# Optimization experiments

Measured on AMD Instinct MI355X. Metric: run time of the kernel, lower is better.

Reference implementation:

```python
import jax, jax.numpy as jnp
import numpy as np

N_HEAD = 16


def setup_inputs() -> dict:
    key = jax.random.key(0)
    ks = jax.random.split(key, 9)
    B, T, C = 4, 2048, 1024
    s = 1.0 / np.sqrt(C)
    x = jax.random.normal(ks[0], (B, T, C), dtype=jnp.float32)
    Wq = jax.random.normal(ks[1], (C, C), dtype=jnp.float32) * s
    bq = jax.random.normal(ks[2], (C,), dtype=jnp.float32) * 0.01
    Wk = jax.random.normal(ks[3], (C, C), dtype=jnp.float32) * s
    bk = jax.random.normal(ks[4], (C,), dtype=jnp.float32) * 0.01
    Wv = jax.random.normal(ks[5], (C, C), dtype=jnp.float32) * s
    bv = jax.random.normal(ks[6], (C,), dtype=jnp.float32) * 0.01
    Wp = jax.random.normal(ks[7], (C, C), dtype=jnp.float32) * s
    bp = jax.random.normal(ks[8], (C,), dtype=jnp.float32) * 0.01
    return {"x": x, "Wq": Wq, "bq": bq, "Wk": Wk, "bk": bk,
            "Wv": Wv, "bv": bv, "Wp": Wp, "bp": bp}


def reference(x, Wq, bq, Wk, bk, Wv, bv, Wp, bp):
    B, T, C = x.shape
    H = N_HEAD
    d = C // H
    # projections (torch Linear: x @ W.T + b)
    q = (x @ Wq.T + bq).reshape(B, T, H, d)  # [B,T,H,d]
    k = (x @ Wk.T + bk).reshape(B, T, H, d)
    v = (x @ Wv.T + bv).reshape(B, T, H, d)
    scale = 1.0 / jnp.sqrt(jnp.asarray(d, dtype=x.dtype))
    # scores: [B,H,T,T]
    att = jnp.einsum('bqhd,bkhd->bhqk', q, k) * scale
    causal = jnp.tril(jnp.ones((T, T), dtype=bool))  # [T,T]
    att = jnp.where(causal[None, None], att, jnp.asarray(-jnp.inf, dtype=att.dtype))
    att = jax.nn.softmax(att, axis=-1)
    y = jnp.einsum('bhqk,bkhd->bqhd', att, v).reshape(B, T, C)
    return y @ Wp.T + bp
```

## Files before the change

### kernel.cpp

```cpp
#include <hip/hip_runtime.h>
#include <hip/hip_bf16.h>

typedef __attribute__((ext_vector_type(8))) short bf16x8;
typedef __attribute__((ext_vector_type(4))) float f32x4;

static constexpr int Tt = 2048;
static constexpr int Cc = 1024;
static constexpr int Dd = 64;
static constexpr int Mm = 8192;

static constexpr size_t XN = (size_t)Mm * Cc;
static constexpr size_t WN = (size_t)Cc * Cc;

__device__ __forceinline__ void async_copy16(void* lds, const void* g) {
  __builtin_amdgcn_global_load_lds(
      (const __attribute__((address_space(1))) void*)g,
      (__attribute__((address_space(3))) void*)lds, 16, 0, 0);
}

__device__ __forceinline__ unsigned short f2bf(float f) {
  union { float f; unsigned int u; } v; v.f = f;
  unsigned int r = (v.u + 0x7fffu + ((v.u >> 16) & 1u)) >> 16;
  return (unsigned short)r;
}
__device__ __forceinline__ unsigned int pack2bf(float f0, float f1) {
  unsigned int b0 = __float_as_uint(f0) + 0x8000u;
  unsigned int b1 = __float_as_uint(f1) + 0x8000u;
  return (b1 & 0xffff0000u) | (b0 >> 16);
}
__device__ __forceinline__ uint4 ldconv_f32(const float* p) {
  float4 lo = *(const float4*)p;
  float4 hi = *(const float4*)(p + 4);
  uint4 r;
  r.x = pack2bf(lo.x, lo.y);
  r.y = pack2bf(lo.z, lo.w);
  r.z = pack2bf(hi.x, hi.y);
  r.w = pack2bf(hi.z, hi.w);
  return r;
}

__global__ __launch_bounds__(256) void convert_all(
    const float* __restrict__ x, const float* __restrict__ wq,
    const float* __restrict__ wk, const float* __restrict__ wv,
    unsigned short* __restrict__ dst)
{
  const size_t i = ((size_t)blockIdx.x * 256 + threadIdx.x) * 8;
  const float* s; size_t off;
  if (i < XN)                { s = x;  off = 0; }
  else if (i < XN + WN)      { s = wq; off = XN; }
  else if (i < XN + 2 * WN)  { s = wk; off = XN + WN; }
  else                       { s = wv; off = XN + 2 * WN; }
  *(uint4*)(dst + i) = ldconv_f32(s + (i - off));
}

template <int MODE>
__device__ __forceinline__ void gemm_async_body(
    unsigned short* As, unsigned short* Bs,
    const unsigned short* __restrict__ A,
    const unsigned short* __restrict__ Bt,
    const float* __restrict__ bias,
    unsigned short* __restrict__ out, float mult)
{
  const int tid  = threadIdx.x;
  const int wave = tid >> 6;
  const int lane = tid & 63;
  const int m16  = lane & 15;
  const int quad = lane >> 4;
  const int row0 = blockIdx.x * 128;
  const int col0 = blockIdx.y * 128;
  const int wm = (wave >> 1) * 64;
  const int wn = (wave & 1) * 64;

  f32x4 acc[4][4] = {};

  const int c0 = tid, c1 = 256 + tid;
  const unsigned short* Ag0 = A  + (size_t)(row0 + (c0 >> 2)) * Cc + (c0 & 3) * 8;
  const unsigned short* Ag1 = A  + (size_t)(row0 + (c1 >> 2)) * Cc + (c1 & 3) * 8;
  const unsigned short* Bg0 = Bt + (size_t)(col0 + (c0 >> 2)) * Cc + (c0 & 3) * 8;
  const unsigned short* Bg1 = Bt + (size_t)(col0 + (c1 >> 2)) * Cc + (c1 & 3) * 8;
  char* Al0 = (char*)As + wave * 1024;
  char* Al1 = (char*)As + 4096 + wave * 1024;
  char* Bl0 = (char*)Bs + wave * 1024;
  char* Bl1 = (char*)Bs + 4096 + wave * 1024;

  for (int k0 = 0; k0 < Cc; k0 += 32) {
    __syncthreads();
    async_copy16(Al0, Ag0 + k0);
    async_copy16(Al1, Ag1 + k0);
    async_copy16(Bl0, Bg0 + k0);
    async_copy16(Bl1, Bg1 + k0);
    __syncthreads();
    bf16x8 af[4], bfr[4];
#pragma unroll
    for (int i = 0; i < 4; ++i)
      af[i] = *(const bf16x8*)(As + (wm + i * 16 + m16) * 32 + quad * 8);
#pragma unroll
    for (int j = 0; j < 4; ++j)
      bfr[j] = *(const bf16x8*)(Bs + (wn + j * 16 + m16) * 32 + quad * 8);
#pragma unroll
    for (int i = 0; i < 4; ++i)
#pragma unroll
      for (int j = 0; j < 4; ++j)
        acc[i][j] = __builtin_amdgcn_mfma_f32_16x16x32_bf16(af[i], bfr[j], acc[i][j], 0, 0, 0);
  }

#pragma unroll
  for (int i = 0; i < 4; ++i) {
    const int rbase = row0 + wm + i * 16 + quad * 4;
#pragma unroll
    for (int j = 0; j < 4; ++j) {
      const int col = col0 + wn + j * 16 + m16;
      const float bv = bias[col];
      if (MODE == 0) {
#pragma unroll
        for (int r = 0; r < 4; ++r)
          out[(size_t)(rbase + r) * Cc + col] = f2bf((acc[i][j][r] + bv) * mult);
      } else {
        const int t0 = rbase & (Tt - 1);
        const int b  = rbase >> 11;
        ushort4 pk;
        pk.x = f2bf(acc[i][j][0] + bv);
        pk.y = f2bf(acc[i][j][1] + bv);
        pk.z = f2bf(acc[i][j][2] + bv);
        pk.w = f2bf(acc[i][j][3] + bv);
        *(ushort4*)(out + (size_t)(b * Cc + col) * Tt + t0) = pk;
      }
    }
  }
}

__global__ __launch_bounds__(256) void qkv_gemm(
    const unsigned short* __restrict__ Xb,
    const unsigned short* __restrict__ Wqb, const float* __restrict__ bq,
    const unsigned short* __restrict__ Wkb, const float* __restrict__ bk,
    const unsigned short* __restrict__ Wvb, const float* __restrict__ bv,
    unsigned short* Qw, unsigned short* Kw, unsigned short* Vtw)
{
  __shared__ __align__(16) unsigned short smem[8192];
  const int z = blockIdx.z;
  if (z == 0)      gemm_async_body<0>(smem, smem + 4096, Xb, Wqb, bq, Qw, 0.125f * 1.44269504f);
  else if (z == 1) gemm_async_body<0>(smem, smem + 4096, Xb, Wkb, bk, Kw, 1.0f);
  else             gemm_async_body<1>(smem, smem + 4096, Xb, Wvb, bv, Vtw, 1.0f);
}

__global__ __launch_bounds__(256) void attn_pair(
    const unsigned short* __restrict__ Q,
    const unsigned short* __restrict__ Kg,
    const unsigned short* __restrict__ Vt,
    unsigned short* __restrict__ Y)
{
  __shared__ __align__(16) unsigned short KV[2 * 8192];

  const int tid  = threadIdx.x;
  const int wave = tid >> 6;
  const int lane = tid & 63;
  const int m16  = lane & 15;
  const int quad = lane >> 4;

  const int p  = blockIdx.x;
  const int bh = blockIdx.y;
  const int b = bh >> 4, h = bh & 15;

  const unsigned short* Kb = Kg + (size_t)(b * Tt) * Cc + h * Dd;
  const unsigned short* Vb = Vt + (size_t)(b * Cc + h * Dd) * Tt;

  const int maxH = 32 - 2 * p;
  const int TOT  = 34;
  const int chp  = quad ^ ((m16 >> 1) & 3);
  const int slA  = m16 + ((quad & 1) << 5);
  const int slB  = slA + 16;
  const int hi   = quad >> 1;

  int kkS[2], rrS[2], chdS[2];
#pragma unroll
  for (int ii = 0; ii < 2; ++ii) {
    const int cc = ii * 256 + tid;
    kkS[ii]  = cc >> 8;
    rrS[ii]  = (cc >> 2) & 63;
    chdS[ii] = (cc & 3) ^ ((rrS[ii] >> 1) & 3);
  }

  int sidx = 63 - 4 * p - wave;
  int qw = sidx * 32;
  int nk = (sidx >> 1) + 1;
  bf16x8 qf[2][2];
  {
    const unsigned short* Qb = Q + (size_t)(b * Tt + qw) * Cc + h * Dd;
#pragma unroll
    for (int s = 0; s < 2; ++s)
#pragma unroll
      for (int kk = 0; kk < 2; ++kk)
        qf[s][kk] = *(const bf16x8*)(Qb + (size_t)(s * 16 + m16) * Cc + kk * 32 + quad * 8);
  }
  f32x4 o[2][4] = {};
  float lsum[2] = {};

  auto writeout = [&](int qw_) {
#pragma unroll
    for (int s = 0; s < 2; ++s) {
      float l = lsum[s];
      l += __shfl_xor(l, 16, 64);
      l += __shfl_xor(l, 32, 64);
      const float inv = (l > 0.f) ? (1.0f / l) : 0.f;
      const int t = qw_ + s * 16 + m16;
      unsigned short* yp = Y + (size_t)(b * Tt + t) * Cc + h * Dd + quad * 4;
#pragma unroll
      for (int jn = 0; jn < 4; ++jn) {
        ushort4 pk;
        pk.x = f2bf(o[s][jn][0] * inv);
        pk.y = f2bf(o[s][jn][1] * inv);
        pk.z = f2bf(o[s][jn][2] * inv);
        pk.w = f2bf(o[s][jn][3] * inv);
        *(ushort4*)(yp + jn * 16) = pk;
      }
    }
  };

  {
    char* KbufB = (char*)KV;
    char* VbufB = KbufB + 8192;
#pragma unroll
    for (int ii = 0; ii < 2; ++ii) {
      async_copy16(KbufB + ii * 4096 + wave * 1024,
                   Kb + (size_t)rrS[ii] * Cc + kkS[ii] * 32 + chdS[ii] * 8);
      async_copy16(VbufB + ii * 4096 + wave * 1024,
                   Vb + (size_t)rrS[ii] * Tt + kkS[ii] * 32 + chdS[ii] * 8);
    }
  }

  for (int g = 0; g < TOT; ++g) {
    if (g == maxH) {
      writeout(qw);
      sidx = 4 * p + wave;
      qw = sidx * 32;
      nk = (sidx >> 1) + 1;
      const unsigned short* Qb = Q + (size_t)(b * Tt + qw) * Cc + h * Dd;
#pragma unroll
      for (int s = 0; s < 2; ++s) {
#pragma unroll
        for (int kk = 0; kk < 2; ++kk)
          qf[s][kk] = *(const bf16x8*)(Qb + (size_t)(s * 16 + m16) * Cc + kk * 32 + quad * 8);
#pragma unroll
        for (int jn = 0; jn < 4; ++jn)
          o[s][jn] = f32x4{0.f, 0.f, 0.f, 0.f};
        lsum[s] = 0.f;
      }
    }
    const int kt  = (g < maxH) ? g : g - maxH;
    const int k0  = kt * 64;
    const int buf = g & 1;

    __syncthreads();
    if (g + 1 < TOT) {
      const int g1  = g + 1;
      const int kt1 = (g1 < maxH) ? g1 : g1 - maxH;
      const int k1  = kt1 * 64;
      char* KbufB = (char*)KV + (buf ^ 1) * 16384;
      char* VbufB = KbufB + 8192;
#pragma unroll
      for (int ii = 0; ii < 2; ++ii) {
        async_copy16(KbufB + ii * 4096 + wave * 1024,
                     Kb + (size_t)(k1 + rrS[ii]) * Cc + kkS[ii] * 32 + chdS[ii] * 8);
        async_copy16(VbufB + ii * 4096 + wave * 1024,
                     Vb + (size_t)rrS[ii] * Tt + k1 + kkS[ii] * 32 + chdS[ii] * 8);
      }
    }

    if (kt < nk) {
      const unsigned short* Kbuf = KV + buf * 8192;
      const unsigned short* Vbuf = Kbuf + 4096;
      bf16x8 kf[2][4], vf[2][4];
#pragma unroll
      for (int kk = 0; kk < 2; ++kk)
#pragma unroll
        for (int jn = 0; jn < 4; ++jn) {
          kf[kk][jn] = *(const bf16x8*)(Kbuf + kk * 2048 + (jn * 16 + m16) * 32 + chp * 8);
          vf[kk][jn] = *(const bf16x8*)(Vbuf + kk * 2048 + (jn * 16 + m16) * 32 + chp * 8);
        }

#pragma unroll
      for (int s = 0; s < 2; ++s) {
        const int smin = qw + s * 16;
        if (k0 > smin + 15) continue;
        f32x4 sv[4] = {};
#pragma unroll
        for (int kk = 0; kk < 2; ++kk)
#pragma unroll
          for (int jn = 0; jn < 4; ++jn)
            sv[jn] = __builtin_amdgcn_mfma_f32_16x16x32_bf16(kf[kk][jn], qf[s][kk], sv[jn], 0, 0, 0);

        if (k0 + 63 <= smin) {
#pragma unroll
          for (int jn = 0; jn < 4; ++jn)
#pragma unroll
            for (int r = 0; r < 4; ++r) {
              const float pv = __builtin_exp2f(sv[jn][r]);
              sv[jn][r] = pv;
              lsum[s] += pv;
            }
        } else {
          const int qcol = smin + m16;
#pragma unroll
          for (int jn = 0; jn < 4; ++jn)
#pragma unroll
            for (int r = 0; r < 4; ++r) {
              const bool masked = (k0 + jn * 16 + quad * 4 + r > qcol);
              const float pv = masked ? 0.f : __builtin_exp2f(sv[jn][r]);
              sv[jn][r] = pv;
              lsum[s] += pv;
            }
        }
        unsigned int P2[4][2];
#pragma unroll
        for (int jn = 0; jn < 4; ++jn) {
          P2[jn][0] = pack2bf(sv[jn][0], sv[jn][1]);
          P2[jn][1] = pack2bf(sv[jn][2], sv[jn][3]);
        }
#pragma unroll
        for (int kk = 0; kk < 2; ++kk) {
          const int a0 = __shfl((int)P2[2 * kk][0],     slA, 64);
          const int b0 = __shfl((int)P2[2 * kk + 1][0], slA, 64);
          const int a1 = __shfl((int)P2[2 * kk][1],     slA, 64);
          const int b1 = __shfl((int)P2[2 * kk + 1][1], slA, 64);
          const int a2 = __shfl((int)P2[2 * kk][0],     slB, 64);
          const int b2 = __shfl((int)P2[2 * kk + 1][0], slB, 64);
          const int a3 = __shfl((int)P2[2 * kk][1],     slB, 64);
          const int b3 = __shfl((int)P2[2 * kk + 1][1], slB, 64);
          uint4 u;
          u.x = (unsigned int)(hi ? b0 : a0);
          u.y = (unsigned int)(hi ? b1 : a1);
          u.z = (unsigned int)(hi ? b2 : a2);
          u.w = (unsigned int)(hi ? b3 : a3);
          union { uint4 u4; bf16x8 bf; } cv; cv.u4 = u;
#pragma unroll
          for (int jn = 0; jn < 4; ++jn)
            o[s][jn] = __builtin_amdgcn_mfma_f32_16x16x32_bf16(vf[kk][jn], cv.bf, o[s][jn], 0, 0, 0);
        }
      }
    }
  }

  writeout(qw);
}

__global__ __launch_bounds__(256) void proj_gemm(
    const unsigned short* __restrict__ Y,
    const float* __restrict__ Wp, const float* __restrict__ bp,
    float* __restrict__ out)
{
  __shared__ __align__(16) unsigned short As[4096];
  __shared__ __align__(16) unsigned short Bs[4096];
  const int tid  = threadIdx.x;
  const int wave = tid >> 6;
  const int lane = tid & 63;
  const int m16  = lane & 15;
  const int quad = lane >> 4;
  const int row0 = blockIdx.x * 128;
  const int col0 = blockIdx.y * 128;
  const int wm = (wave >> 1) * 64;
  const int wn = (wave & 1) * 64;

  f32x4 acc[4][4] = {};

  const int c0 = tid, c1 = 256 + tid;
  const unsigned short* Ag0 = Y + (size_t)(row0 + (c0 >> 2)) * Cc + (c0 & 3) * 8;
  const unsigned short* Ag1 = Y + (size_t)(row0 + (c1 >> 2)) * Cc + (c1 & 3) * 8;
  const float* Bg0 = Wp + (size_t)(col0 + (c0 >> 2)) * Cc + (c0 & 3) * 8;
  const float* Bg1 = Wp + (size_t)(col0 + (c1 >> 2)) * Cc + (c1 & 3) * 8;
  char* Al0 = (char*)As + wave * 1024;
  char* Al1 = (char*)As + 4096 + wave * 1024;

  uint4 b0 = ldconv_f32(Bg0);
  uint4 b1 = ldconv_f32(Bg1);

  for (int k0 = 0; k0 < Cc; k0 += 32) {
    __syncthreads();
    async_copy16(Al0, Ag0 + k0);
    async_copy16(Al1, Ag1 + k0);
    *(uint4*)(Bs + (size_t)c0 * 8) = b0;
    *(uint4*)(Bs + (size_t)c1 * 8) = b1;
    __syncthreads();
    if (k0 + 32 < Cc) {
      b0 = ldconv_f32(Bg0 + k0 + 32);
      b1 = ldconv_f32(Bg1 + k0 + 32);
    }
    bf16x8 af[4], bfr[4];
#pragma unroll
    for (int i = 0; i < 4; ++i)
      af[i] = *(const bf16x8*)(As + (wm + i * 16 + m16) * 32 + quad * 8);
#pragma unroll
    for (int j = 0; j < 4; ++j)
      bfr[j] = *(const bf16x8*)(Bs + (wn + j * 16 + m16) * 32 + quad * 8);
#pragma unroll
    for (int i = 0; i < 4; ++i)
#pragma unroll
      for (int j = 0; j < 4; ++j)
        acc[i][j] = __builtin_amdgcn_mfma_f32_16x16x32_bf16(af[i], bfr[j], acc[i][j], 0, 0, 0);
  }

#pragma unroll
  for (int i = 0; i < 4; ++i) {
    const int rbase = row0 + wm + i * 16 + quad * 4;
#pragma unroll
    for (int j = 0; j < 4; ++j) {
      const int col = col0 + wn + j * 16 + m16;
      const float bv = bp[col];
#pragma unroll
      for (int r = 0; r < 4; ++r)
        out[(size_t)(rbase + r) * Cc + col] = acc[i][j][r] + bv;
    }
  }
}

extern "C" void kernel_launch(void* const* d_in, const int* in_sizes, int n_in,
                              void* d_out, int out_size, void* d_ws, size_t ws_size,
                              hipStream_t stream)
{
  const float* x  = (const float*)d_in[0];
  const float* Wq = (const float*)d_in[1];
  const float* bq = (const float*)d_in[2];
  const float* Wk = (const float*)d_in[3];
  const float* bk = (const float*)d_in[4];
  const float* Wv = (const float*)d_in[5];
  const float* bv = (const float*)d_in[6];
  const float* Wp = (const float*)d_in[7];
  const float* bp = (const float*)d_in[8];

  unsigned short* ws  = (unsigned short*)d_ws;
  unsigned short* Qw  = ws;
  unsigned short* Kw  = ws + (size_t)1 * XN;
  unsigned short* Vtw = ws + (size_t)2 * XN;
  unsigned short* Yw  = ws + (size_t)3 * XN;

  unsigned short* cvt = (unsigned short*)d_out;
  unsigned short* Xb  = cvt;
  unsigned short* Wqb = cvt + XN;
  unsigned short* Wkb = cvt + XN + WN;
  unsigned short* Wvb = cvt + XN + 2 * WN;
  float* out = (float*)d_out;

  convert_all<<<5632, 256, 0, stream>>>(x, Wq, Wk, Wv, cvt);
  qkv_gemm<<<dim3(64, 8, 3), 256, 0, stream>>>(Xb, Wqb, bq, Wkb, bk, Wvb, bv, Qw, Kw, Vtw);
  attn_pair<<<dim3(8, 64), 256, 0, stream>>>(Qw, Kw, Vtw, Yw);
  proj_gemm<<<dim3(64, 8), 256, 0, stream>>>(Yw, Wp, bp, out);
}
```

Before: 300.3 us.

## Replace paired causal attention blocks with per-strip blocks and permlane swaps

Each attention block previously handled a heavy and a light query strip pair in sequence (34 iterations). Now each block handles one strip, with 16 blocks per head launched largest-first. This gives more blocks for occupancy and removes the mid-loop strip switch. The P-matrix transpose now uses permlane32/16 swap intrinsics instead of eight shuffles plus selects. The row-sum uses a small vector accumulator, and launch bounds request 4 blocks per CU. The trade-off is uneven per-block work, which now relies on the hardware scheduler to balance the causal triangle.

```diff
diff --git a/kernel.cpp b/kernel.cpp
--- a/kernel.cpp
+++ b/kernel.cpp
@@ -143,7 +143,7 @@
   else             gemm_async_body<1>(smem, smem + 4096, Xb, Wvb, bv, Vtw, 1.0f);
 }
 
-__global__ __launch_bounds__(256) void attn_pair(
+__global__ __launch_bounds__(256, 4) void attn_strip(
     const unsigned short* __restrict__ Q,
     const unsigned short* __restrict__ Kg,
     const unsigned short* __restrict__ Vt,
@@ -157,19 +157,19 @@
   const int m16  = lane & 15;
   const int quad = lane >> 4;
 
-  const int p  = blockIdx.x;
+  const int pp = 15 - blockIdx.x;
   const int bh = blockIdx.y;
   const int b = bh >> 4, h = bh & 15;
 
   const unsigned short* Kb = Kg + (size_t)(b * Tt) * Cc + h * Dd;
   const unsigned short* Vb = Vt + (size_t)(b * Cc + h * Dd) * Tt;
 
-  const int maxH = 32 - 2 * p;
-  const int TOT  = 34;
+  const int sidx = 4 * pp + wave;
+  const int qw   = sidx * 32;
+  const int nk   = (sidx >> 1) + 1;
+  const int TOT  = 2 * pp + 2;
+
   const int chp  = quad ^ ((m16 >> 1) & 3);
-  const int slA  = m16 + ((quad & 1) << 5);
-  const int slB  = slA + 16;
-  const int hi   = quad >> 1;
 
   int kkS[2], rrS[2], chdS[2];
 #pragma unroll
@@ -180,9 +180,6 @@
     chdS[ii] = (cc & 3) ^ ((rrS[ii] >> 1) & 3);
   }
 
-  int sidx = 63 - 4 * p - wave;
-  int qw = sidx * 32;
-  int nk = (sidx >> 1) + 1;
   bf16x8 qf[2][2];
   {
     const unsigned short* Qb = Q + (size_t)(b * Tt + qw) * Cc + h * Dd;
@@ -194,27 +191,6 @@
   }
   f32x4 o[2][4] = {};
   float lsum[2] = {};
-
-  auto writeout = [&](int qw_) {
-#pragma unroll
-    for (int s = 0; s < 2; ++s) {
-      float l = lsum[s];
-      l += __shfl_xor(l, 16, 64);
-      l += __shfl_xor(l, 32, 64);
-      const float inv = (l > 0.f) ? (1.0f / l) : 0.f;
-      const int t = qw_ + s * 16 + m16;
-      unsigned short* yp = Y + (size_t)(b * Tt + t) * Cc + h * Dd + quad * 4;
-#pragma unroll
-      for (int jn = 0; jn < 4; ++jn) {
-        ushort4 pk;
-        pk.x = f2bf(o[s][jn][0] * inv);
-        pk.y = f2bf(o[s][jn][1] * inv);
-        pk.z = f2bf(o[s][jn][2] * inv);
-        pk.w = f2bf(o[s][jn][3] * inv);
-        *(ushort4*)(yp + jn * 16) = pk;
-      }
-    }
-  };
 
   {
     char* KbufB = (char*)KV;
@@ -229,32 +205,12 @@
   }
 
   for (int g = 0; g < TOT; ++g) {
-    if (g == maxH) {
-      writeout(qw);
-      sidx = 4 * p + wave;
-      qw = sidx * 32;
-      nk = (sidx >> 1) + 1;
-      const unsigned short* Qb = Q + (size_t)(b * Tt + qw) * Cc + h * Dd;
-#pragma unroll
-      for (int s = 0; s < 2; ++s) {
-#pragma unroll
-        for (int kk = 0; kk < 2; ++kk)
-          qf[s][kk] = *(const bf16x8*)(Qb + (size_t)(s * 16 + m16) * Cc + kk * 32 + quad * 8);
-#pragma unroll
-        for (int jn = 0; jn < 4; ++jn)
-          o[s][jn] = f32x4{0.f, 0.f, 0.f, 0.f};
-        lsum[s] = 0.f;
-      }
-    }
-    const int kt  = (g < maxH) ? g : g - maxH;
-    const int k0  = kt * 64;
+    const int k0  = g * 64;
     const int buf = g & 1;
 
     __syncthreads();
     if (g + 1 < TOT) {
-      const int g1  = g + 1;
-      const int kt1 = (g1 < maxH) ? g1 : g1 - maxH;
-      const int k1  = kt1 * 64;
+      const int k1 = (g + 1) * 64;
       char* KbufB = (char*)KV + (buf ^ 1) * 16384;
       char* VbufB = KbufB + 8192;
 #pragma unroll
@@ -266,7 +222,7 @@
       }
     }
 
-    if (kt < nk) {
+    if (g < nk) {
       const unsigned short* Kbuf = KV + buf * 8192;
       const unsigned short* Vbuf = Kbuf + 4096;
       bf16x8 kf[2][4], vf[2][4];
@@ -289,6 +245,7 @@
           for (int jn = 0; jn < 4; ++jn)
             sv[jn] = __builtin_amdgcn_mfma_f32_16x16x32_bf16(kf[kk][jn], qf[s][kk], sv[jn], 0, 0, 0);
 
+        f32x4 lacc = {0.f, 0.f, 0.f, 0.f};
         if (k0 + 63 <= smin) {
 #pragma unroll
           for (int jn = 0; jn < 4; ++jn)
@@ -296,7 +253,7 @@
             for (int r = 0; r < 4; ++r) {
               const float pv = __builtin_exp2f(sv[jn][r]);
               sv[jn][r] = pv;
-              lsum[s] += pv;
+              lacc[r] += pv;
             }
         } else {
           const int qcol = smin + m16;
@@ -307,9 +264,11 @@
               const bool masked = (k0 + jn * 16 + quad * 4 + r > qcol);
               const float pv = masked ? 0.f : __builtin_exp2f(sv[jn][r]);
               sv[jn][r] = pv;
-              lsum[s] += pv;
+              lacc[r] += pv;
             }
         }
+        lsum[s] += (lacc[0] + lacc[1]) + (lacc[2] + lacc[3]);
+
         unsigned int P2[4][2];
 #pragma unroll
         for (int jn = 0; jn < 4; ++jn) {
@@ -318,19 +277,15 @@
         }
 #pragma unroll
         for (int kk = 0; kk < 2; ++kk) {
-          const int a0 = __shfl((int)P2[2 * kk][0],     slA, 64);
-          const int b0 = __shfl((int)P2[2 * kk + 1][0], slA, 64);
-          const int a1 = __shfl((int)P2[2 * kk][1],     slA, 64);
-          const int b1 = __shfl((int)P2[2 * kk + 1][1], slA, 64);
-          const int a2 = __shfl((int)P2[2 * kk][0],     slB, 64);
-          const int b2 = __shfl((int)P2[2 * kk + 1][0], slB, 64);
-          const int a3 = __shfl((int)P2[2 * kk][1],     slB, 64);
-          const int b3 = __shfl((int)P2[2 * kk + 1][1], slB, 64);
+          auto r0 = __builtin_amdgcn_permlane32_swap(P2[2 * kk][0], P2[2 * kk + 1][0], false, false);
+          auto t0 = __builtin_amdgcn_permlane16_swap(r0[0], r0[1], false, false);
+          auto r1 = __builtin_amdgcn_permlane32_swap(P2[2 * kk][1], P2[2 * kk + 1][1], false, false);
+          auto t1 = __builtin_amdgcn_permlane16_swap(r1[0], r1[1], false, false);
           uint4 u;
-          u.x = (unsigned int)(hi ? b0 : a0);
-          u.y = (unsigned int)(hi ? b1 : a1);
-          u.z = (unsigned int)(hi ? b2 : a2);
-          u.w = (unsigned int)(hi ? b3 : a3);
+          u.x = t0[0];
+          u.y = t1[0];
+          u.z = t0[1];
+          u.w = t1[1];
           union { uint4 u4; bf16x8 bf; } cv; cv.u4 = u;
 #pragma unroll
           for (int jn = 0; jn < 4; ++jn)
@@ -340,7 +295,24 @@
     }
   }
 
-  writeout(qw);
+#pragma unroll
+  for (int s = 0; s < 2; ++s) {
+    float l = lsum[s];
+    l += __shfl_xor(l, 16, 64);
+    l += __shfl_xor(l, 32, 64);
+    const float inv = (l > 0.f) ? (1.0f / l) : 0.f;
+    const int t = qw + s * 16 + m16;
+    unsigned short* yp = Y + (size_t)(b * Tt + t) * Cc + h * Dd + quad * 4;
+#pragma unroll
+    for (int jn = 0; jn < 4; ++jn) {
+      ushort4 pk;
+      pk.x = f2bf(o[s][jn][0] * inv);
+      pk.y = f2bf(o[s][jn][1] * inv);
+      pk.z = f2bf(o[s][jn][2] * inv);
+      pk.w = f2bf(o[s][jn][3] * inv);
+      *(ushort4*)(yp + jn * 16) = pk;
+    }
+  }
 }
 
 __global__ __launch_bounds__(256) void proj_gemm(
@@ -441,6 +413,6 @@
 
   convert_all<<<5632, 256, 0, stream>>>(x, Wq, Wk, Wv, cvt);
   qkv_gemm<<<dim3(64, 8, 3), 256, 0, stream>>>(Xb, Wqb, bq, Wkb, bk, Wvb, bv, Qw, Kw, Vtw);
-  attn_pair<<<dim3(8, 64), 256, 0, stream>>>(Qw, Kw, Vtw, Yw);
+  attn_strip<<<dim3(16, 64), 256, 0, stream>>>(Qw, Kw, Vtw, Yw);
   proj_gemm<<<dim3(64, 8), 256, 0, stream>>>(Yw, Wp, bp, out);
 }
```

New measurement: 473.6 us. +57.7%, slower.
